# Kernel tuning notes

Measured on AMD Instinct MI355X. Metric: run time of the kernel, lower is better.

## Reference

```python
import jax, jax.numpy as jnp
import numpy as np

B, W, C, C2, K_DIV = 4, 64, 256, 256, 8
DPROJ = C // K_DIV  # 32


def setup_inputs() -> dict:
    key = jax.random.key(0)
    k1, k2, k3, k4 = jax.random.split(key, 4)
    x = jax.random.normal(k1, (B, W, W, C), dtype=jnp.float32)
    input_h = jax.random.normal(k2, (B, W, W, C2), dtype=jnp.float32)
    f_w = jax.random.normal(k3, (1, 1, C2, DPROJ), dtype=jnp.float32) * 0.05
    g_w = jax.random.normal(k4, (1, 1, C, DPROJ), dtype=jnp.float32) * 0.05
    return {"x": x, "input_h": input_h, "f_w": f_w, "g_w": g_w}


def reference(x, input_h, f_w, g_w):
    b, w, _, c = x.shape
    c2 = input_h.shape[-1]
    # 1x1 convs == channel matmuls
    f = jnp.einsum('bhwc,cd->bhwd', input_h, f_w[0, 0])   # [B,W,W,Dp]
    g = jnp.einsum('bhwc,cd->bhwd', x, g_w[0, 0])          # [B,W,W,Dp]
    gf = g.reshape(b, w * w, -1)                            # [B,N,Dp]
    ff = f.reshape(b, w * w, -1)                            # [B,N,Dp]
    s = jnp.einsum('bnd,bmd->bnm', gf, ff)                  # unscaled QK^T
    beta = jax.nn.softmax(s, axis=-1)
    hf = input_h.reshape(b, w * w, c2)                      # [B,N,C2]
    o = jnp.einsum('bnm,bmc->bnc', beta, hf).reshape(b, w, w, c2)
    return jnp.concatenate([o, x], axis=-1)                 # [B,W,W,C2+C]
```

## Files before the change

kernel.cpp:

```cpp
#include <hip/hip_runtime.h>
#include <hip/hip_bf16.h>

#define NB   4
#define NROW 4096
#define CIN  256
#define OUTC 512
#define DP   32
#define LOG2E 1.4426950408889634f

typedef __bf16 bf16x8 __attribute__((ext_vector_type(8)));
typedef float  f32x4  __attribute__((ext_vector_type(4)));
typedef float  f32x16 __attribute__((ext_vector_type(16)));
typedef ushort ushort8 __attribute__((ext_vector_type(8)));

#define MFMA32(a, b, c) __builtin_amdgcn_mfma_f32_32x32x16_bf16((a), (b), (c), 0, 0, 0)

__device__ __forceinline__ ushort f2bf(float x) {
  union { float f; unsigned u; } v; v.f = x;
  unsigned r = v.u + 0x7fffu + ((v.u >> 16) & 1u);
  return (ushort)(r >> 16);
}

__device__ __forceinline__ uint pack2(float a, float b) {
  __hip_bfloat162 h = __float22bfloat162_rn(float2{a, b});
  uint u; __builtin_memcpy(&u, &h, 4);
  return u;
}

__device__ __forceinline__ bf16x8 mk8(uint a, uint b, uint c, uint d) {
  uint tmp[4] = {a, b, c, d};
  bf16x8 r; __builtin_memcpy(&r, tmp, 16);
  return r;
}

__device__ __forceinline__ void gload_lds16(const void* g, void* l) {
  __builtin_amdgcn_global_load_lds(
      (const __attribute__((address_space(1))) unsigned int*)g,
      (__attribute__((address_space(3))) unsigned int*)l, 16, 0, 0);
}


__global__ __launch_bounds__(256) void proj_mfma(
    const float* __restrict__ x, const float* __restrict__ h,
    const float* __restrict__ fw, const float* __restrict__ gw,
    ushort* __restrict__ Qb, ushort* __restrict__ Kb, ushort* __restrict__ Vw) {
  __shared__ ushort Ab[64 * 256];
  __shared__ ushort Wt[32 * 256];
  const int t = threadIdx.x;
  const int which = blockIdx.y;
  const float* in   = which ? h : x;
  const float* wsrc = which ? fw : gw;
  ushort* dst = which ? Kb : Qb;
  const float qsc = which ? 1.f : LOG2E;
  const int row0 = blockIdx.x * 64;

  {
    const float4* inp = (const float4*)(in + (size_t)row0 * CIN);
#pragma unroll
    for (int i = 0; i < 16; ++i) {
      const int idx = i * 256 + t;
      const int r = idx >> 6;
      const int c = (idx & 63) * 4;
      const float4 v = inp[idx];
      ushort tmp[4] = {f2bf(v.x), f2bf(v.y), f2bf(v.z), f2bf(v.w)};
      const int slot = (c >> 3) ^ (r & 7);
      *(uint2*)&Ab[r * 256 + (slot << 3) + (c & 7)] = *(const uint2*)tmp;
    }
  }
  {
    const int d = t & 31;
    const int k0 = (t >> 5) * 32;
#pragma unroll 8
    for (int j = 0; j < 32; ++j)
      Wt[d * 256 + k0 + j] = f2bf(wsrc[(size_t)(k0 + j) * DP + d]);
  }
  __syncthreads();

  const int w = t >> 6, l = t & 63, lo = l & 15, hi = l >> 4;
  f32x4 acc[2];
  acc[0] = (f32x4){0.f, 0.f, 0.f, 0.f};
  acc[1] = (f32x4){0.f, 0.f, 0.f, 0.f};
  const int R = w * 16 + lo;
#pragma unroll
  for (int kk = 0; kk < 8; ++kk) {
    const int slot = (kk * 4 + hi) ^ (R & 7);
    const bf16x8 a = *(const bf16x8*)&Ab[R * 256 + (slot << 3)];
#pragma unroll
    for (int nt = 0; nt < 2; ++nt) {
      const bf16x8 bfr = *(const bf16x8*)&Wt[(nt * 16 + lo) * 256 + kk * 32 + hi * 8];
      acc[nt] = __builtin_amdgcn_mfma_f32_16x16x32_bf16(a, bfr, acc[nt], 0, 0, 0);
    }
  }
#pragma unroll
  for (int nt = 0; nt < 2; ++nt)
#pragma unroll
    for (int r = 0; r < 4; ++r)
      dst[(size_t)(row0 + w * 16 + hi * 4 + r) * DP + nt * 16 + lo] =
          f2bf(acc[nt][r] * qsc);

  if (which) {
    const int b = row0 >> 12;
    const int tile = (row0 & 4095) >> 6;
    const int c = t;
    const int cs = (c + (c >> 3)) & 7;
    ushort* vdst = Vw + ((size_t)(b * 64 + tile) * 256 + c) * 64;
#pragma unroll
    for (int g = 0; g < 8; ++g) {
      ushort tmp[8];
#pragma unroll
      for (int j = 0; j < 8; ++j) {
        const int slot = (c >> 3) ^ j;
        tmp[j] = Ab[(8 * g + j) * 256 + (slot << 3) + (c & 7)];
      }
      *(ushort8*)(vdst + ((g ^ cs) << 3)) = *(const ushort8*)tmp;
    }
  }
}

__global__ __launch_bounds__(256, 2) void attn32f(
    const ushort* __restrict__ Qb, const ushort* __restrict__ Kb,
    const ushort* __restrict__ Vw, float* __restrict__ pml,
    ushort* __restrict__ pacc) {
  __shared__ ushort Vt[16384];

  const int t  = threadIdx.x;
  const int w  = t >> 6;
  const int l  = t & 63;
  const int qq = l & 31;
  const int h  = l >> 5;

  const int bid = blockIdx.x;
  const int s   = bid & 3;
  const int b   = (bid >> 2) & 3;
  const int q0  = (bid >> 4) * 128 + w * 32;
  const size_t rbase = (size_t)b * NROW;

  bf16x8 qf[2];
#pragma unroll
  for (int ks = 0; ks < 2; ++ks)
    qf[ks] = *(const bf16x8*)(Qb + (rbase + q0 + qq) * DP + ks * 16 + h * 8);

  f32x16 acc[8];
#pragma unroll
  for (int i = 0; i < 8; ++i) acc[i] = (f32x16){};
  float mrow = -1e30f, lsum = 0.f;

  const int tI0 = s * 16;

  {
    const ushort* src = Vw + (size_t)(b * 64 + tI0) * 16384;
#pragma unroll
    for (int i = 0; i < 8; ++i)
      gload_lds16(src + (w * 8 + i) * 512 + l * 8, &Vt[(w * 8 + i) * 512]);
  }
  bf16x8 kf[2][2];
#pragma unroll
  for (int e = 0; e < 2; ++e)
#pragma unroll
    for (int ks = 0; ks < 2; ++ks)
      kf[e][ks] = *(const bf16x8*)(Kb + (rbase + tI0 * 64 + e * 32 + qq) * DP +
                                   ks * 16 + h * 8);

  for (int tt = 0; tt < 16; ++tt) {
    f32x16 st0 = (f32x16){}, st1 = (f32x16){};
    st0 = MFMA32(kf[0][0], qf[0], st0);
    st0 = MFMA32(kf[0][1], qf[1], st0);
    st1 = MFMA32(kf[1][0], qf[0], st1);
    st1 = MFMA32(kf[1][1], qf[1], st1);

    float m4 = st0[0];
#pragma unroll
    for (int i = 1; i < 16; ++i) m4 = fmaxf(m4, st0[i]);
#pragma unroll
    for (int i = 0; i < 16; ++i) m4 = fmaxf(m4, st1[i]);
    m4 = fmaxf(m4, __shfl_xor(m4, 32, 64));
    if (__any(m4 > mrow + 7.f)) {
      const float mn = fmaxf(mrow, m4);
      const float alpha = exp2f(mrow - mn);
      mrow = mn;
#pragma unroll
      for (int ct = 0; ct < 8; ++ct) acc[ct] *= alpha;
      lsum *= alpha;
    }
    float ps = 0.f;
#pragma unroll
    for (int i = 0; i < 16; ++i) {
      const float p = exp2f(st0[i] - mrow); st0[i] = p; ps += p;
    }
#pragma unroll
    for (int i = 0; i < 16; ++i) {
      const float p = exp2f(st1[i] - mrow); st1[i] = p; ps += p;
    }
    ps += __shfl_xor(ps, 32, 64);
    lsum += ps;

    bf16x8 pb[4];
    {
      const uint a00 = pack2(st0[0],  st0[1]),  a01 = pack2(st0[2],  st0[3]);
      const uint a10 = pack2(st0[4],  st0[5]),  a11 = pack2(st0[6],  st0[7]);
      const uint a20 = pack2(st0[8],  st0[9]),  a21 = pack2(st0[10], st0[11]);
      const uint a30 = pack2(st0[12], st0[13]), a31 = pack2(st0[14], st0[15]);
      auto s0 = __builtin_amdgcn_permlane32_swap(a00, a10, false, false);
      auto s1 = __builtin_amdgcn_permlane32_swap(a01, a11, false, false);
      auto s2 = __builtin_amdgcn_permlane32_swap(a20, a30, false, false);
      auto s3 = __builtin_amdgcn_permlane32_swap(a21, a31, false, false);
      pb[0] = mk8(s0[0], s1[0], s0[1], s1[1]);
      pb[1] = mk8(s2[0], s3[0], s2[1], s3[1]);
      const uint b00 = pack2(st1[0],  st1[1]),  b01 = pack2(st1[2],  st1[3]);
      const uint b10 = pack2(st1[4],  st1[5]),  b11 = pack2(st1[6],  st1[7]);
      const uint b20 = pack2(st1[8],  st1[9]),  b21 = pack2(st1[10], st1[11]);
      const uint b30 = pack2(st1[12], st1[13]), b31 = pack2(st1[14], st1[15]);
      auto s4 = __builtin_amdgcn_permlane32_swap(b00, b10, false, false);
      auto s5 = __builtin_amdgcn_permlane32_swap(b01, b11, false, false);
      auto s6 = __builtin_amdgcn_permlane32_swap(b20, b30, false, false);
      auto s7 = __builtin_amdgcn_permlane32_swap(b21, b31, false, false);
      pb[2] = mk8(s4[0], s5[0], s4[1], s5[1]);
      pb[3] = mk8(s6[0], s7[0], s6[1], s7[1]);
    }

    if (tt < 15) {
      const size_t kb = rbase + (size_t)(tI0 + tt + 1) * 64;
#pragma unroll
      for (int e = 0; e < 2; ++e)
#pragma unroll
        for (int ks = 0; ks < 2; ++ks)
          kf[e][ks] = *(const bf16x8*)(Kb + (kb + e * 32 + qq) * DP + ks * 16 + h * 8);
    }

    __syncthreads();

    __builtin_amdgcn_s_setprio(1);
#pragma unroll
    for (int ct = 0; ct < 8; ++ct) {
      const int c = ct * 32 + qq;
      const int cs = (c + (c >> 3)) & 7;
#pragma unroll
      for (int kt = 0; kt < 4; ++kt) {
        const bf16x8 v = *(const bf16x8*)&Vt[c * 64 + ((((kt << 1) + h) ^ cs) << 3)];
        acc[ct] = MFMA32(v, pb[kt], acc[ct]);
      }
    }
    __builtin_amdgcn_s_setprio(0);

    __syncthreads();

    if (tt < 15) {
      const ushort* src = Vw + (size_t)(b * 64 + tI0 + tt + 1) * 16384;
#pragma unroll
      for (int i = 0; i < 8; ++i)
        gload_lds16(src + (w * 8 + i) * 512 + l * 8, &Vt[(w * 8 + i) * 512]);
    }
  }

  const size_t prow = rbase + q0 + qq;
  if (h == 0) {
    float* mlp = pml + (prow * 4 + s) * 2;
    mlp[0] = mrow;
    mlp[1] = lsum;
  }
  ushort* pr = pacc + (prow * 4 + s) * 256;
#pragma unroll
  for (int ct = 0; ct < 8; ++ct)
#pragma unroll
    for (int j = 0; j < 4; ++j) {
      uint2 d;
      d.x = pack2(acc[ct][4 * j], acc[ct][4 * j + 1]);
      d.y = pack2(acc[ct][4 * j + 2], acc[ct][4 * j + 3]);
      *(uint2*)&pr[ct * 32 + j * 8 + h * 4] = d;
    }
}

__global__ __launch_bounds__(256) void reduce_concat(
    const float* __restrict__ pml, const ushort* __restrict__ pacc,
    const float* __restrict__ x, float* __restrict__ out) {
  const int t = threadIdx.x;
  const int row = blockIdx.x * 8 + (t >> 5);
  const int c0 = (t & 31) * 8;

  float ms[4], ls[4];
  float m = -1e30f;
#pragma unroll
  for (int s = 0; s < 4; ++s) {
    ms[s] = pml[((size_t)row * 4 + s) * 2];
    ls[s] = pml[((size_t)row * 4 + s) * 2 + 1];
    m = fmaxf(m, ms[s]);
  }
  float L = 0.f, wgt[4];
#pragma unroll
  for (int s = 0; s < 4; ++s) {
    wgt[s] = exp2f(ms[s] - m);
    L += wgt[s] * ls[s];
  }
  float o[8] = {0.f, 0.f, 0.f, 0.f, 0.f, 0.f, 0.f, 0.f};
#pragma unroll
  for (int s = 0; s < 4; ++s) {
    const bf16x8 a = *(const bf16x8*)(pacc + ((size_t)row * 4 + s) * 256 + c0);
    const float wg = wgt[s];
#pragma unroll
    for (int i = 0; i < 8; ++i) o[i] += wg * (float)a[i];
  }
  const float inv = 1.f / L;
  float4 o0 = {o[0] * inv, o[1] * inv, o[2] * inv, o[3] * inv};
  float4 o1 = {o[4] * inv, o[5] * inv, o[6] * inv, o[7] * inv};
  float4* op = (float4*)(out + (size_t)row * OUTC + c0);
  op[0] = o0; op[1] = o1;
  const float4* xp = (const float4*)(x + (size_t)row * CIN + c0);
  float4* oc = (float4*)(out + (size_t)row * OUTC + 256 + c0);
  oc[0] = xp[0]; oc[1] = xp[1];
}

__global__ __launch_bounds__(256) void proj_fb(
    const float* __restrict__ x, const float* __restrict__ h,
    const float* __restrict__ fw, const float* __restrict__ gw,
    float* __restrict__ out) {
  __shared__ float wl[8192];
  __shared__ float rows[8][260];
  const int t = threadIdx.x;
  const int which = blockIdx.y;
  const float* in = which ? h : x;
  const float* w  = which ? fw : gw;
  for (int i = t; i < 8192; i += 256) wl[i] = w[i];
  const int row0 = blockIdx.x * 32;
  const int d = t & 31, rl = t >> 5;
  for (int rp = 0; rp < 4; ++rp) {
    __syncthreads();
    for (int i = t; i < 2048; i += 256)
      rows[i >> 8][i & 255] = in[(long)(row0 + rp * 8 + (i >> 8)) * CIN + (i & 255)];
    __syncthreads();
    float a = 0.f;
#pragma unroll 8
    for (int c = 0; c < 256; ++c) a = fmaf(rows[rl][c], wl[c * 32 + d], a);
    const long row = row0 + rp * 8 + rl;
    ((ushort*)(out + row * OUTC + 256))[which * 32 + d] = f2bf(a);
  }
}

__global__ __launch_bounds__(256) void attn_fb(
    const float* __restrict__ h, float* __restrict__ out) {
  __shared__ alignas(16) ushort Vt[256][72];
  __shared__ alignas(16) ushort Pl[4][16][72];
  const int t = threadIdx.x;
  const int w = t >> 6, l = t & 63, lo = l & 15, hi = l >> 4;
  const int bid = blockIdx.x;
  const int b = (bid >> 1) & 3;
  const int qb = ((bid >> 3) << 1) | (bid & 1);
  const int q0 = qb * 64;
  const long rowbase = (long)b * NROW;
  const ushort* gslot = (const ushort*)(out + (rowbase + q0 + w * 16 + lo) * OUTC + 256);
  const bf16x8 qf = *(const bf16x8*)(gslot + hi * 8);
  f32x4 acc[16];
#pragma unroll
  for (int i = 0; i < 16; ++i) acc[i] = (f32x4){0.f, 0.f, 0.f, 0.f};
  float mrow[4] = {-1e30f, -1e30f, -1e30f, -1e30f};
  float lsum[4] = {0.f, 0.f, 0.f, 0.f};
  for (int k0 = 0; k0 < NROW; k0 += 64) {
    bf16x8 kf[4];
#pragma unroll
    for (int kt = 0; kt < 4; ++kt) {
      const ushort* fslot =
          (const ushort*)(out + (rowbase + k0 + kt * 16 + lo) * OUTC + 256) + 32;
      kf[kt] = *(const bf16x8*)(fslot + hi * 8);
    }
    __syncthreads();
    {
      const float* hp = h + (rowbase + k0) * CIN + t;
#pragma unroll
      for (int g8 = 0; g8 < 8; ++g8) {
        ushort tmp[8];
#pragma unroll
        for (int i = 0; i < 8; ++i) tmp[i] = f2bf(hp[(g8 * 8 + i) * CIN]);
        *(bf16x8*)&Vt[t][g8 * 8] = *(const bf16x8*)tmp;
      }
    }
    __syncthreads();
    f32x4 sv[4];
#pragma unroll
    for (int kt = 0; kt < 4; ++kt)
      sv[kt] = __builtin_amdgcn_mfma_f32_16x16x32_bf16(
          qf, kf[kt], (f32x4){0.f, 0.f, 0.f, 0.f}, 0, 0, 0);
    float alpha[4];
    bool upd = false;
#pragma unroll
    for (int r = 0; r < 4; ++r) {
      float m4 = fmaxf(fmaxf(sv[0][r], sv[1][r]), fmaxf(sv[2][r], sv[3][r]));
#pragma unroll
      for (int off = 1; off < 16; off <<= 1) m4 = fmaxf(m4, __shfl_xor(m4, off, 64));
      const float mn = fmaxf(mrow[r], m4);
      alpha[r] = __expf(mrow[r] - mn);
      upd |= (mn > mrow[r]);
      mrow[r] = mn;
    }
    if (__any(upd)) {
#pragma unroll
      for (int ct = 0; ct < 16; ++ct)
#pragma unroll
        for (int r = 0; r < 4; ++r) acc[ct][r] *= alpha[r];
#pragma unroll
      for (int r = 0; r < 4; ++r) lsum[r] *= alpha[r];
    }
#pragma unroll
    for (int r = 0; r < 4; ++r) {
      float ps = 0.f;
#pragma unroll
      for (int kt = 0; kt < 4; ++kt) {
        const float p = __expf(sv[kt][r] - mrow[r]);
        sv[kt][r] = p;
        ps += p;
      }
#pragma unroll
      for (int off = 1; off < 16; off <<= 1) ps += __shfl_xor(ps, off, 64);
      lsum[r] += ps;
    }
#pragma unroll
    for (int kt = 0; kt < 4; ++kt)
#pragma unroll
      for (int r = 0; r < 4; ++r)
        Pl[w][hi * 4 + r][kt * 16 + lo] = f2bf(sv[kt][r]);
    asm volatile("s_waitcnt lgkmcnt(0)" ::: "memory");
    const bf16x8 pa0 = *(const bf16x8*)&Pl[w][lo][hi * 8];
    const bf16x8 pa1 = *(const bf16x8*)&Pl[w][lo][32 + hi * 8];
#pragma unroll
    for (int ct = 0; ct < 16; ++ct) {
      const bf16x8 v0 = *(const bf16x8*)&Vt[ct * 16 + lo][hi * 8];
      const bf16x8 v1 = *(const bf16x8*)&Vt[ct * 16 + lo][32 + hi * 8];
      acc[ct] = __builtin_amdgcn_mfma_f32_16x16x32_bf16(pa0, v0, acc[ct], 0, 0, 0);
      acc[ct] = __builtin_amdgcn_mfma_f32_16x16x32_bf16(pa1, v1, acc[ct], 0, 0, 0);
    }
  }
#pragma unroll
  for (int r = 0; r < 4; ++r) {
    const float inv = 1.f / lsum[r];
    float* orow = out + (rowbase + q0 + w * 16 + hi * 4 + r) * OUTC;
#pragma unroll
    for (int ct = 0; ct < 16; ++ct) orow[ct * 16 + lo] = acc[ct][r] * inv;
  }
}

__global__ __launch_bounds__(256) void concat_fb(
    const float4* __restrict__ x, float4* __restrict__ out) {
  const int idx = blockIdx.x * 256 + threadIdx.x;
  const int row = idx >> 6, c4 = idx & 63;
  out[row * 128 + 64 + c4] = x[idx];
}

extern "C" void kernel_launch(void* const* d_in, const int* in_sizes, int n_in,
                              void* d_out, int out_size, void* d_ws, size_t ws_size,
                              hipStream_t stream) {
  const float* x  = (const float*)d_in[0];
  const float* h  = (const float*)d_in[1];
  const float* fw = (const float*)d_in[2];
  const float* gw = (const float*)d_in[3];
  float* out = (float*)d_out;

  const size_t rows = (size_t)NB * NROW;
  const size_t base = 10ull * 1024 * 1024;
  const size_t need = base + rows * 4 * 8 + rows * 4 * 512;

  if (ws_size >= need) {
    ushort* Qw = (ushort*)d_ws;
    ushort* Kw = Qw + (1ull << 19);
    ushort* Vw = Kw + (1ull << 19);
    float*  pml  = (float*)((char*)d_ws + base);
    ushort* pacc = (ushort*)((char*)d_ws + base + rows * 4 * 8);

    proj_mfma<<<dim3(256, 2), 256, 0, stream>>>(x, h, fw, gw, Qw, Kw, Vw);
    attn32f<<<512, 256, 0, stream>>>(Qw, Kw, Vw, pml, pacc);
    reduce_concat<<<2048, 256, 0, stream>>>(pml, pacc, x, out);
  } else {
    proj_fb<<<dim3(512, 2), 256, 0, stream>>>(x, h, fw, gw, out);
    attn_fb<<<256, 256, 0, stream>>>(h, out);
    concat_fb<<<4096, 256, 0, stream>>>((const float4*)x, (float4*)out);
  }
}
```

Measured before the change: 89.83 us.

## Double-buffer V tiles in LDS and relayout V for constant-offset reads

Allocates two LDS buffers for the V tile and issues the asynchronous global-to-LDS load for the next tile at the top of each iteration, so the load overlaps the QK and softmax math and one barrier per iteration goes away. The V producer now writes V in a layout where each lane's MFMA operand sits at a fixed per-lane base plus compile-time offsets, which removes the per-access swizzle arithmetic. The row max and sum reductions become tree reductions to shorten the dependency chains. Doubling the LDS to 64KB per block may limit how many blocks fit on a CU, which could cut into the two-blocks-per-CU launch bound.

```diff
diff --git a/kernel.cpp b/kernel.cpp
--- a/kernel.cpp
+++ b/kernel.cpp
@@ -102,18 +102,20 @@
     const int b = row0 >> 12;
     const int tile = (row0 & 4095) >> 6;
     const int c = t;
-    const int cs = (c + (c >> 3)) & 7;
-    ushort* vdst = Vw + ((size_t)(b * 64 + tile) * 256 + c) * 64;
-#pragma unroll
-    for (int g = 0; g < 8; ++g) {
-      ushort tmp[8];
-#pragma unroll
-      for (int j = 0; j < 8; ++j) {
-        const int slot = (c >> 3) ^ j;
-        tmp[j] = Ab[(8 * g + j) * 256 + (slot << 3) + (c & 7)];
+    ushort* vdst = Vw + (size_t)(b * 64 + tile) * 16384;
+#pragma unroll
+    for (int kt = 0; kt < 4; ++kt)
+#pragma unroll
+      for (int s2 = 0; s2 < 2; ++s2) {
+        const int kbase = 16 * kt + 8 * (s2 ^ (c & 1));
+        ushort tmp[8];
+#pragma unroll
+        for (int j = 0; j < 8; ++j) {
+          const int slot = (c >> 3) ^ j;
+          tmp[j] = Ab[(kbase + j) * 256 + (slot << 3) + (c & 7)];
+        }
+        *(ushort8*)(vdst + kt * 4096 + c * 16 + s2 * 8) = *(const ushort8*)tmp;
       }
-      *(ushort8*)(vdst + ((g ^ cs) << 3)) = *(const ushort8*)tmp;
-    }
   }
 }
 
@@ -121,7 +123,7 @@
     const ushort* __restrict__ Qb, const ushort* __restrict__ Kb,
     const ushort* __restrict__ Vw, float* __restrict__ pml,
     ushort* __restrict__ pacc) {
-  __shared__ ushort Vt[16384];
+  __shared__ ushort Vt[2][16384];
 
   const int t  = threadIdx.x;
   const int w  = t >> 6;
@@ -146,12 +148,13 @@
   float mrow = -1e30f, lsum = 0.f;
 
   const int tI0 = s * 16;
+  const int vlane = qq * 32 + ((h ^ (qq & 1)) << 4);
 
   {
     const ushort* src = Vw + (size_t)(b * 64 + tI0) * 16384;
 #pragma unroll
     for (int i = 0; i < 8; ++i)
-      gload_lds16(src + (w * 8 + i) * 512 + l * 8, &Vt[(w * 8 + i) * 512]);
+      gload_lds16(src + (w * 8 + i) * 512 + l * 8, &Vt[0][(w * 8 + i) * 512]);
   }
   bf16x8 kf[2][2];
 #pragma unroll
@@ -160,39 +163,56 @@
     for (int ks = 0; ks < 2; ++ks)
       kf[e][ks] = *(const bf16x8*)(Kb + (rbase + tI0 * 64 + e * 32 + qq) * DP +
                                    ks * 16 + h * 8);
+  __syncthreads();
+  int cur = 0;
 
   for (int tt = 0; tt < 16; ++tt) {
+    if (tt < 15) {
+      const ushort* src = Vw + (size_t)(b * 64 + tI0 + tt + 1) * 16384;
+      ushort* dstl = &Vt[cur ^ 1][0];
+#pragma unroll
+      for (int i = 0; i < 8; ++i)
+        gload_lds16(src + (w * 8 + i) * 512 + l * 8, dstl + (w * 8 + i) * 512);
+    }
+
     f32x16 st0 = (f32x16){}, st1 = (f32x16){};
     st0 = MFMA32(kf[0][0], qf[0], st0);
     st0 = MFMA32(kf[0][1], qf[1], st0);
     st1 = MFMA32(kf[1][0], qf[0], st1);
     st1 = MFMA32(kf[1][1], qf[1], st1);
 
-    float m4 = st0[0];
-#pragma unroll
-    for (int i = 1; i < 16; ++i) m4 = fmaxf(m4, st0[i]);
-#pragma unroll
-    for (int i = 0; i < 16; ++i) m4 = fmaxf(m4, st1[i]);
-    m4 = fmaxf(m4, __shfl_xor(m4, 32, 64));
-    if (__any(m4 > mrow + 7.f)) {
-      const float mn = fmaxf(mrow, m4);
-      const float alpha = exp2f(mrow - mn);
-      mrow = mn;
-#pragma unroll
-      for (int ct = 0; ct < 8; ++ct) acc[ct] *= alpha;
-      lsum *= alpha;
-    }
-    float ps = 0.f;
-#pragma unroll
-    for (int i = 0; i < 16; ++i) {
-      const float p = exp2f(st0[i] - mrow); st0[i] = p; ps += p;
-    }
-#pragma unroll
-    for (int i = 0; i < 16; ++i) {
-      const float p = exp2f(st1[i] - mrow); st1[i] = p; ps += p;
-    }
-    ps += __shfl_xor(ps, 32, 64);
-    lsum += ps;
+    {
+      float mx[16];
+#pragma unroll
+      for (int i = 0; i < 16; ++i) mx[i] = fmaxf(st0[i], st1[i]);
+#pragma unroll
+      for (int d = 8; d >= 1; d >>= 1)
+#pragma unroll
+        for (int i = 0; i < d; ++i) mx[i] = fmaxf(mx[i], mx[i + d]);
+      const float m4 = fmaxf(mx[0], __shfl_xor(mx[0], 32, 64));
+      if (__any(m4 > mrow + 7.f)) {
+        const float mn = fmaxf(mrow, m4);
+        const float alpha = exp2f(mrow - mn);
+        mrow = mn;
+#pragma unroll
+        for (int ct = 0; ct < 8; ++ct) acc[ct] *= alpha;
+        lsum *= alpha;
+      }
+    }
+#pragma unroll
+    for (int i = 0; i < 16; ++i) st0[i] = exp2f(st0[i] - mrow);
+#pragma unroll
+    for (int i = 0; i < 16; ++i) st1[i] = exp2f(st1[i] - mrow);
+    {
+      float sm[16];
+#pragma unroll
+      for (int i = 0; i < 16; ++i) sm[i] = st0[i] + st1[i];
+#pragma unroll
+      for (int d = 8; d >= 1; d >>= 1)
+#pragma unroll
+        for (int i = 0; i < d; ++i) sm[i] += sm[i + d];
+      lsum += sm[0] + __shfl_xor(sm[0], 32, 64);
+    }
 
     bf16x8 pb[4];
     {
@@ -227,29 +247,20 @@
           kf[e][ks] = *(const bf16x8*)(Kb + (kb + e * 32 + qq) * DP + ks * 16 + h * 8);
     }
 
-    __syncthreads();
-
+    const char* vb = (const char*)&Vt[cur][0] + vlane;
     __builtin_amdgcn_s_setprio(1);
 #pragma unroll
     for (int ct = 0; ct < 8; ++ct) {
-      const int c = ct * 32 + qq;
-      const int cs = (c + (c >> 3)) & 7;
 #pragma unroll
       for (int kt = 0; kt < 4; ++kt) {
-        const bf16x8 v = *(const bf16x8*)&Vt[c * 64 + ((((kt << 1) + h) ^ cs) << 3)];
+        const bf16x8 v = *(const bf16x8*)(vb + kt * 8192 + ct * 1024);
         acc[ct] = MFMA32(v, pb[kt], acc[ct]);
       }
     }
     __builtin_amdgcn_s_setprio(0);
 
     __syncthreads();
-
-    if (tt < 15) {
-      const ushort* src = Vw + (size_t)(b * 64 + tI0 + tt + 1) * 16384;
-#pragma unroll
-      for (int i = 0; i < 8; ++i)
-        gload_lds16(src + (w * 8 + i) * 512 + l * 8, &Vt[(w * 8 + i) * 512]);
-    }
+    cur ^= 1;
   }
 
   const size_t prow = rbase + q0 + qq;
```

After: 89.54 us. No clear change (-0.3%).
